# Optimization experiments

Hardware: AMD Instinct MI355X
Metric: run time of the kernel (lower is better)

The kernel has to match this reference:

```python
import jax, jax.numpy as jnp
import numpy as np

B, L, V, E, H2, M, OOV = 128, 400, 50000, 512, 1024, 1024, 50


def setup_inputs() -> dict:
    key = jax.random.key(0)
    ks = jax.random.split(key, 14)
    s = 0.02
    return {
        "y": jax.random.randint(ks[0], (B,), 0, V),
        "h": jax.random.normal(ks[1], (1, B, H2), jnp.float32),
        "memory_bank": jax.random.normal(ks[2], (B, L, M), jnp.float32),
        "src_mask": jnp.ones((B, L), jnp.float32),
        "max_num_oovs": OOV,
        "src_oov": jax.random.randint(ks[3], (B, L), 0, V + OOV),
        # learned parameters (PyTorch Linear y = x @ W + b with W stored [in, out])
        "emb": jax.random.normal(ks[4], (V, E), jnp.float32) * s,
        "W_ih": jax.random.normal(ks[5], (E, 3 * H2), jnp.float32) * s,   # GRU input weights (r|z|n)
        "W_hh": jax.random.normal(ks[6], (H2, 3 * H2), jnp.float32) * s,  # GRU hidden weights (r|z|n)
        "b_ih": jnp.zeros((3 * H2,), jnp.float32),
        "b_hh": jnp.zeros((3 * H2,), jnp.float32),
        "W_mem": jax.random.normal(ks[7], (M, H2), jnp.float32) * s,      # attention memory_project (no bias)
        "W_dec": jax.random.normal(ks[8], (H2, H2), jnp.float32) * s,     # attention decode_project
        "b_dec": jnp.zeros((H2,), jnp.float32),
        "v": jax.random.normal(ks[9], (H2,), jnp.float32) * s,            # attention score vector (no bias)
        "W_pgen": jax.random.normal(ks[10], (M + H2 + E, 1), jnp.float32) * s,
        "b_pgen": jnp.zeros((1,), jnp.float32),
        "W_v1": jax.random.normal(ks[11], (M + H2, H2), jnp.float32) * s,
        "b_v1": jnp.zeros((H2,), jnp.float32),
        "W_v2": jax.random.normal(ks[12], (H2, V), jnp.float32) * s,
        "b_v2": jnp.zeros((V,), jnp.float32),
    }


def reference(y, h, memory_bank, src_mask, max_num_oovs, src_oov,
              emb, W_ih, W_hh, b_ih, b_hh, W_mem, W_dec, b_dec, v,
              W_pgen, b_pgen, W_v1, b_v1, W_v2, b_v2):
    # --- embedding lookup (single decode step) ---
    y_emb = emb[y]                                    # [B, E]
    h0 = h[-1]                                        # [B, H2]

    # --- one-step GRU (PyTorch gate order r, z, n); dropout is identity (eval) ---
    gi = y_emb @ W_ih + b_ih                          # [B, 3*H2]
    gh = h0 @ W_hh + b_hh
    i_r, i_z, i_n = jnp.split(gi, 3, axis=-1)
    h_r, h_z, h_n = jnp.split(gh, 3, axis=-1)
    r = jax.nn.sigmoid(i_r + h_r)
    z = jax.nn.sigmoid(i_z + h_z)
    n = jnp.tanh(i_n + r * h_n)
    h_next = (1.0 - z) * n + z * h0                   # [B, H2]

    # --- concat (Bahdanau) attention with masked softmax ---
    enc_feat = jnp.einsum('blm,mh->blh', memory_bank, W_mem)   # [B, L, H2]
    dec_feat = h_next @ W_dec + b_dec                           # [B, H2]
    scores = jnp.tanh(enc_feat + dec_feat[:, None, :]) @ v     # [B, L]
    attn = jax.nn.softmax(scores, axis=1) * src_mask
    attn_dist = attn / attn.sum(axis=1, keepdims=True)         # renormalized masked softmax
    context = jnp.einsum('bl,blm->bm', attn_dist, memory_bank) # [B, M]

    # --- vocab distribution ---
    vd_in = jnp.concatenate([context, h_next], axis=1)          # [B, M+H2]
    logits = (vd_in @ W_v1 + b_v1) @ W_v2 + b_v2                # [B, V]
    vocab_dist = jax.nn.softmax(logits, axis=1)

    # --- generation gate ---
    pg_in = jnp.concatenate([context, h_next, y_emb], axis=1)   # [B, M+H2+E]
    p_gen = jax.nn.sigmoid(pg_in @ W_pgen + b_pgen)             # [B, 1]

    # --- copy mechanism: scatter attention mass into extended vocab ---
    vocab_dist_ = p_gen * vocab_dist
    attn_dist_ = (1.0 - p_gen) * attn_dist
    bsz = vocab_dist_.shape[0]
    if max_num_oovs > 0:
        vocab_dist_ = jnp.concatenate(
            [vocab_dist_, jnp.zeros((bsz, max_num_oovs), vocab_dist_.dtype)], axis=1)
    rows = jnp.arange(bsz)[:, None]
    final_dist = vocab_dist_.at[rows, src_oov].add(attn_dist_)  # [B, V+OOV]

    return final_dist, h_next[None], context, attn_dist, p_gen
```

## Files before the change

### kernel.cpp

```cpp
#include <hip/hip_runtime.h>

#define B_   128
#define L_   400
#define V_   50000
#define E_   512
#define H2_  1024
#define M_   1024
#define OOV_ 50
#define VE_  50050
#define BL_  51200

typedef __attribute__((ext_vector_type(8))) short short8;
typedef __attribute__((ext_vector_type(4))) float f32x4;

__device__ __forceinline__ unsigned short f2bf(float f){
  unsigned int u = __builtin_bit_cast(unsigned int, f);
  u = (u + 0x7FFFu + ((u >> 16) & 1u)) >> 16;
  return (unsigned short)u;
}
__device__ __forceinline__ float bf2f(unsigned short s){
  unsigned int u = ((unsigned int)s) << 16;
  return __builtin_bit_cast(float, u);
}

__device__ __forceinline__ void gl_lds16(const void* g, void* l){
  __builtin_amdgcn_global_load_lds(
      (const __attribute__((address_space(1))) unsigned int*)g,
      (__attribute__((address_space(3))) unsigned int*)l, 16, 0, 0);
}

__device__ __forceinline__ float wredsum(float v){
  #pragma unroll
  for (int o = 32; o > 0; o >>= 1) v += __shfl_xor(v, o);
  return v;
}
__device__ __forceinline__ float wredmax(float v){
  #pragma unroll
  for (int o = 32; o > 0; o >>= 1) v = fmaxf(v, __shfl_xor(v, o));
  return v;
}

__global__ void embed_gather_kernel(const int* __restrict__ y, const float* __restrict__ emb,
                                    float* __restrict__ yemb){
  int idx = blockIdx.x * 256 + threadIdx.x;
  int b  = idx >> 7;
  int c4 = (idx & 127) << 2;
  float4 v = *(const float4*)(emb + (size_t)y[b] * E_ + c4);
  *(float4*)(yemb + (size_t)b * E_ + c4) = v;
}

__global__ void mb_convert_kernel(const float* __restrict__ mb, unsigned char* __restrict__ mbT){
  int u = blockIdx.x * 256 + threadIdx.x;
  int gr  = u >> 7;
  int m16 = u & 127;
  const float* src = mb + (size_t)gr * 1024 + m16 * 8;
  float4 f0 = *(const float4*)src;
  float4 f1 = *(const float4*)(src + 4);
  uint4 w;
  w.x = (unsigned)f2bf(f0.x) | ((unsigned)f2bf(f0.y) << 16);
  w.y = (unsigned)f2bf(f0.z) | ((unsigned)f2bf(f0.w) << 16);
  w.z = (unsigned)f2bf(f1.x) | ((unsigned)f2bf(f1.y) << 16);
  w.w = (unsigned)f2bf(f1.z) | ((unsigned)f2bf(f1.w) << 16);
  int panel = gr >> 7, r = gr & 127;
  int ks = m16 >> 3, c16 = m16 & 7;
  size_t dst = (size_t)panel * 262144 + (size_t)ks * 16384
             + (size_t)((r * 128 + c16 * 16) ^ ((r & 7) << 4));
  *(uint4*)(mbT + dst) = w;
}

__global__ void wmem_transposeT_kernel(const float* __restrict__ W, unsigned char* __restrict__ WTt){
  __shared__ float tile[32][33];
  int n0 = blockIdx.x * 32, k0 = blockIdx.y * 32;
  int tx = threadIdx.x, ty = threadIdx.y;
  #pragma unroll
  for (int i = 0; i < 32; i += 8) tile[ty + i][tx] = W[(size_t)(k0 + ty + i) * H2_ + n0 + tx];
  __syncthreads();
  int id = ty * 32 + tx;
  if (id < 128){
    int nn = id & 31, k16 = id >> 5;
    int col = n0 + nn, kb = k0 + k16 * 8;
    uint4 w;
    w.x = (unsigned)f2bf(tile[k16*8+0][nn]) | ((unsigned)f2bf(tile[k16*8+1][nn]) << 16);
    w.y = (unsigned)f2bf(tile[k16*8+2][nn]) | ((unsigned)f2bf(tile[k16*8+3][nn]) << 16);
    w.z = (unsigned)f2bf(tile[k16*8+4][nn]) | ((unsigned)f2bf(tile[k16*8+5][nn]) << 16);
    w.w = (unsigned)f2bf(tile[k16*8+6][nn]) | ((unsigned)f2bf(tile[k16*8+7][nn]) << 16);
    int cpn = col >> 7, r = col & 127;
    int ks = kb >> 6, c16 = (kb & 63) >> 3;
    size_t dst = (size_t)cpn * 262144 + (size_t)ks * 16384
               + (size_t)((r * 128 + c16 * 16) ^ ((r & 7) << 4));
    *(uint4*)(WTt + dst) = w;
  }
}

__launch_bounds__(256)
__global__ void gemm128_kernel(const float* __restrict__ A, int lda,
                               const float* __restrict__ W, int ldw,
                               const float* __restrict__ bias,
                               float* __restrict__ C, int ldc,
                               int N, int kChunk, int addBias)
{
  int tid = threadIdx.x;
  int wv = tid >> 6, lane = tid & 63, lr = lane & 15, lhi = lane >> 4;
  int colBase = blockIdx.x * 128 + wv * 32;
  int colL[2];
  colL[0] = min(colBase + lr, N - 1);
  colL[1] = min(colBase + 16 + lr, N - 1);
  int k0 = blockIdx.y * kChunk;

  f32x4 zero = {0.f, 0.f, 0.f, 0.f};
  f32x4 acc[8][2];
  #pragma unroll
  for (int r = 0; r < 8; r++){ acc[r][0] = zero; acc[r][1] = zero; }

  int nks = kChunk >> 5;
  for (int ks = 0; ks < nks; ++ks){
    int k = k0 + ks * 32 + lhi * 8;
    short8 bf[2];
    #pragma unroll
    for (int cf = 0; cf < 2; cf++){
      #pragma unroll
      for (int j = 0; j < 8; j++)
        bf[cf][j] = (short)f2bf(W[(size_t)(k + j) * ldw + colL[cf]]);
    }
    #pragma unroll
    for (int rf = 0; rf < 8; rf++){
      const float* ap = A + (size_t)(rf * 16 + lr) * lda + k;
      float4 a0 = *(const float4*)ap;
      float4 a1 = *(const float4*)(ap + 4);
      short8 af;
      af[0]=(short)f2bf(a0.x); af[1]=(short)f2bf(a0.y); af[2]=(short)f2bf(a0.z); af[3]=(short)f2bf(a0.w);
      af[4]=(short)f2bf(a1.x); af[5]=(short)f2bf(a1.y); af[6]=(short)f2bf(a1.z); af[7]=(short)f2bf(a1.w);
      acc[rf][0] = __builtin_amdgcn_mfma_f32_16x16x32_bf16(af, bf[0], acc[rf][0], 0, 0, 0);
      acc[rf][1] = __builtin_amdgcn_mfma_f32_16x16x32_bf16(af, bf[1], acc[rf][1], 0, 0, 0);
    }
  }

  bool addB = addBias && (blockIdx.y == 0);
  #pragma unroll
  for (int cf = 0; cf < 2; cf++){
    int col = colBase + cf * 16 + lr;
    bool ok = col < N;
    float bv = addB ? bias[colL[cf]] : 0.f;
    #pragma unroll
    for (int rf = 0; rf < 8; rf++)
      #pragma unroll
      for (int i = 0; i < 4; i++){
        int row = rf * 16 + lhi * 4 + i;
        if (ok) atomicAdd(&C[(size_t)row * ldc + col], acc[rf][cf][i] + bv);
      }
  }
}

__launch_bounds__(256)
__global__ void gemm_v1_kernel(const float* __restrict__ A1, const float* __restrict__ A2,
                               const float* __restrict__ W,
                               const float* __restrict__ bias,
                               float* __restrict__ C, int N, int kChunk)
{
  int tid = threadIdx.x;
  int wv = tid >> 6, lane = tid & 63, lr = lane & 15, lhi = lane >> 4;
  int colBase = blockIdx.x * 128 + wv * 32;
  int halfY = gridDim.y >> 1;
  const float* Asrc = (blockIdx.y < halfY) ? A1 : A2;
  int yk = (blockIdx.y < halfY) ? blockIdx.y : (blockIdx.y - halfY);
  int k0 = yk * kChunk;
  int wk0 = blockIdx.y * kChunk;

  f32x4 zero = {0.f, 0.f, 0.f, 0.f};
  f32x4 acc[8][2];
  #pragma unroll
  for (int r = 0; r < 8; r++){ acc[r][0] = zero; acc[r][1] = zero; }

  int nks = kChunk >> 5;
  for (int ks = 0; ks < nks; ++ks){
    int k  = k0 + ks * 32 + lhi * 8;
    int wk = wk0 + ks * 32 + lhi * 8;
    short8 bf[2];
    #pragma unroll
    for (int cf = 0; cf < 2; cf++){
      #pragma unroll
      for (int j = 0; j < 8; j++)
        bf[cf][j] = (short)f2bf(W[(size_t)(wk + j) * H2_ + colBase + cf * 16 + lr]);
    }
    #pragma unroll
    for (int rf = 0; rf < 8; rf++){
      const float* ap = Asrc + (size_t)(rf * 16 + lr) * 1024 + k;
      float4 a0 = *(const float4*)ap;
      float4 a1 = *(const float4*)(ap + 4);
      short8 af;
      af[0]=(short)f2bf(a0.x); af[1]=(short)f2bf(a0.y); af[2]=(short)f2bf(a0.z); af[3]=(short)f2bf(a0.w);
      af[4]=(short)f2bf(a1.x); af[5]=(short)f2bf(a1.y); af[6]=(short)f2bf(a1.z); af[7]=(short)f2bf(a1.w);
      acc[rf][0] = __builtin_amdgcn_mfma_f32_16x16x32_bf16(af, bf[0], acc[rf][0], 0, 0, 0);
      acc[rf][1] = __builtin_amdgcn_mfma_f32_16x16x32_bf16(af, bf[1], acc[rf][1], 0, 0, 0);
    }
  }

  bool addB = (blockIdx.y == 0);
  #pragma unroll
  for (int cf = 0; cf < 2; cf++){
    int col = colBase + cf * 16 + lr;
    float bv = addB ? bias[col] : 0.f;
    #pragma unroll
    for (int rf = 0; rf < 8; rf++)
      #pragma unroll
      for (int i = 0; i < 4; i++){
        int row = rf * 16 + lhi * 4 + i;
        atomicAdd(&C[(size_t)row * H2_ + col], acc[rf][cf][i] + bv);
      }
  }
}

__launch_bounds__(256)
__global__ void gemm_bfA_kernel(const unsigned short* __restrict__ A,
                                const float* __restrict__ W,
                                const float* __restrict__ bias,
                                float* __restrict__ C0, float* __restrict__ C1,
                                int N, int kChunk)
{
  int tid = threadIdx.x;
  int wv = tid >> 6, lane = tid & 63, lr = lane & 15, lhi = lane >> 4;
  int colBase = blockIdx.x * 128 + wv * 32;
  int colL[2];
  colL[0] = min(colBase + lr, N - 1);
  colL[1] = min(colBase + 16 + lr, N - 1);
  int k0 = blockIdx.y * kChunk;
  float* Cw = (blockIdx.y == 0) ? C0 : C1;

  f32x4 zero = {0.f, 0.f, 0.f, 0.f};
  f32x4 acc[8][2];
  #pragma unroll
  for (int r = 0; r < 8; r++){ acc[r][0] = zero; acc[r][1] = zero; }

  int nks = kChunk >> 5;
  for (int ks = 0; ks < nks; ++ks){
    int k = k0 + ks * 32 + lhi * 8;
    short8 bf[2];
    #pragma unroll
    for (int cf = 0; cf < 2; cf++){
      #pragma unroll
      for (int j = 0; j < 8; j++)
        bf[cf][j] = (short)f2bf(W[(size_t)(k + j) * N + colL[cf]]);
    }
    #pragma unroll
    for (int rf = 0; rf < 8; rf++){
      short8 af = *(const short8*)(A + (size_t)(rf * 16 + lr) * 1024 + k);
      acc[rf][0] = __builtin_amdgcn_mfma_f32_16x16x32_bf16(af, bf[0], acc[rf][0], 0, 0, 0);
      acc[rf][1] = __builtin_amdgcn_mfma_f32_16x16x32_bf16(af, bf[1], acc[rf][1], 0, 0, 0);
    }
  }

  bool addB = (blockIdx.y == 0);
  #pragma unroll
  for (int cf = 0; cf < 2; cf++){
    int col = colBase + cf * 16 + lr;
    bool ok = col < N;
    float bv = addB ? bias[colL[cf]] : 0.f;
    #pragma unroll
    for (int rf = 0; rf < 8; rf++)
      #pragma unroll
      for (int i = 0; i < 4; i++){
        int row = rf * 16 + lhi * 4 + i;
        if (ok) Cw[(size_t)row * V_ + col] = acc[rf][cf][i] + bv;
      }
  }
}

__global__ void gru_gates_kernel(const float* __restrict__ gi, const float* __restrict__ gh,
                                 const float* __restrict__ bih, const float* __restrict__ bhh,
                                 const float* __restrict__ h0, float* __restrict__ hn){
  int idx = blockIdx.x * 256 + threadIdx.x;
  int b = idx >> 10, j = idx & 1023;
  const float* gib = gi + (size_t)b * 3072;
  const float* ghb = gh + (size_t)b * 3072;
  float ir = gib[j]        + bih[j],        hr = ghb[j]        + bhh[j];
  float iz = gib[j + 1024] + bih[j + 1024], hz = ghb[j + 1024] + bhh[j + 1024];
  float in_= gib[j + 2048] + bih[j + 2048], hnv= ghb[j + 2048] + bhh[j + 2048];
  float r = 1.f / (1.f + __expf(-(ir + hr)));
  float z = 1.f / (1.f + __expf(-(iz + hz)));
  float n = tanhf(in_ + r * hnv);
  hn[idx] = (1.f - z) * n + z * h0[idx];
}

__launch_bounds__(512, 3)
__global__ void scores_kernel(const unsigned char* __restrict__ mbT,
                              const unsigned char* __restrict__ WTt,
                              const float* __restrict__ dec, const float* __restrict__ vvec,
                              float* __restrict__ scr)
{
  __shared__ __align__(16) unsigned char LDSm[65536];
  const int tid = threadIdx.x, lane = tid & 63;
  const int wv = tid >> 6, lr = lane & 15, lhi = lane >> 4;
  const int wru = wv >> 2, wcu = wv & 3;

  int p = blockIdx.x;
  int lid = (p & 7) * 400 + (p >> 3);
  int rp = lid >> 3, cp = lid & 7;
  int r0 = rp << 7;

  int wvu = __builtin_amdgcn_readfirstlane(wv);
  const unsigned char* seg = (wvu < 4 ? mbT + (size_t)rp * 262144
                                      : WTt + (size_t)cp * 262144)
                             + (wvu & 3) * 4096 + lane * 16;
  const int segLds = (wvu & 3) * 4096 + (wvu < 4 ? 0 : 16384);

  int aoff[4], boff[2];
  #pragma unroll
  for (int rf = 0; rf < 4; rf++){
    int row = wru * 64 + rf * 16 + lr;
    aoff[rf] = (row * 128 + lhi * 16) ^ ((row & 7) << 4);
  }
  #pragma unroll
  for (int cf = 0; cf < 2; cf++){
    int col = wcu * 32 + cf * 16 + lr;
    boff[cf] = ((col * 128 + lhi * 16) ^ ((col & 7) << 4)) + 16384;
  }

  f32x4 zero = {0.f, 0.f, 0.f, 0.f};
  f32x4 acc[4][2];
  #pragma unroll
  for (int rf = 0; rf < 4; rf++){ acc[rf][0] = zero; acc[rf][1] = zero; }

  #pragma unroll
  for (int j = 0; j < 4; j++)
    gl_lds16(seg + j * 1024, &LDSm[segLds + j * 1024]);

  #pragma unroll 1
  for (int t = 0; t < 16; ++t){
    const int cur = (t & 1) << 15;
    if (t < 15){
      const unsigned char* s = seg + (size_t)(t + 1) * 16384;
      const int nb = ((t + 1) & 1) << 15;
      #pragma unroll
      for (int j = 0; j < 4; j++)
        gl_lds16(s + j * 1024, &LDSm[nb + segLds + j * 1024]);
      asm volatile("s_waitcnt vmcnt(4)" ::: "memory");
    } else {
      asm volatile("s_waitcnt vmcnt(0)" ::: "memory");
    }
    __builtin_amdgcn_sched_barrier(0);
    __builtin_amdgcn_s_barrier();
    __builtin_amdgcn_sched_barrier(0);
    #pragma unroll
    for (int k2 = 0; k2 < 2; k2++){
      short8 af[4], bfr[2];
      #pragma unroll
      for (int rf = 0; rf < 4; rf++) af[rf]  = *(const short8*)&LDSm[cur + (aoff[rf] ^ (k2 << 6))];
      #pragma unroll
      for (int cf = 0; cf < 2; cf++) bfr[cf] = *(const short8*)&LDSm[cur + (boff[cf] ^ (k2 << 6))];
      __builtin_amdgcn_s_setprio(1);
      #pragma unroll
      for (int rf = 0; rf < 4; rf++)
        #pragma unroll
        for (int cf = 0; cf < 2; cf++)
          acc[rf][cf] = __builtin_amdgcn_mfma_f32_16x16x32_bf16(af[rf], bfr[cf], acc[rf][cf], 0, 0, 0);
      __builtin_amdgcn_s_setprio(0);
    }
    __builtin_amdgcn_sched_barrier(0);
    asm volatile("s_waitcnt lgkmcnt(0)" ::: "memory");
    __builtin_amdgcn_s_barrier();
    __builtin_amdgcn_sched_barrier(0);
  }

  int colb = (cp << 7) + wcu * 32 + lr;
  float vv0 = vvec[colb], vv1 = vvec[colb + 16];
  #pragma unroll
  for (int rf = 0; rf < 4; rf++){
    #pragma unroll
    for (int i = 0; i < 4; i++){
      int grow = r0 + wru * 64 + rf * 16 + lhi * 4 + i;
      int bb = grow / 400;
      const float* dp = dec + (size_t)bb * 1024 + colb;
      float x0 = acc[rf][0][i] + dp[0];
      float x1 = acc[rf][1][i] + dp[16];
      float part = (1.f - 2.f / (__expf(2.f * x0) + 1.f)) * vv0
                 + (1.f - 2.f / (__expf(2.f * x1) + 1.f)) * vv1;
      part += __shfl_xor(part, 1);
      part += __shfl_xor(part, 2);
      part += __shfl_xor(part, 4);
      part += __shfl_xor(part, 8);
      if (lr == 0) atomicAdd(&scr[grow], part);
    }
  }
}

__global__ void attn_softmax_kernel(const float* __restrict__ scores, const float* __restrict__ mask,
                                    float* __restrict__ attn){
  int b = blockIdx.x, t = threadIdx.x;
  int wv = t >> 6, lane = t & 63;
  __shared__ float red[4];
  float s0 = (t < 400)       ? scores[b * 400 + t]       : -1e30f;
  float s1 = (t + 256 < 400) ? scores[b * 400 + t + 256] : -1e30f;
  float m = wredmax(fmaxf(s0, s1));
  if (lane == 0) red[wv] = m;
  __syncthreads();
  float M = fmaxf(fmaxf(red[0], red[1]), fmaxf(red[2], red[3]));
  __syncthreads();
  float e0 = (t < 400)       ? __expf(s0 - M) * mask[b * 400 + t]       : 0.f;
  float e1 = (t + 256 < 400) ? __expf(s1 - M) * mask[b * 400 + t + 256] : 0.f;
  float s = wredsum(e0 + e1);
  if (lane == 0) red[wv] = s;
  __syncthreads();
  float inv = 1.f / (red[0] + red[1] + red[2] + red[3]);
  if (t < 400)       attn[b * 400 + t]       = e0 * inv;
  if (t + 256 < 400) attn[b * 400 + t + 256] = e1 * inv;
}

__launch_bounds__(256)
__global__ void context_kernel(const float* __restrict__ attn, const unsigned char* __restrict__ mbT,
                               float* __restrict__ ctx){
  int b = blockIdx.y, lc = blockIdx.x, t = threadIdx.x;
  int u = t & 127;
  int half = t >> 7;
  __shared__ float a[100];
  if (t < 100) a[t] = attn[b * 400 + lc * 100 + t];
  __syncthreads();
  int ks = u >> 3, c16 = u & 7;
  float s[8];
  #pragma unroll
  for (int j = 0; j < 8; j++) s[j] = 0.f;
  for (int l = half; l < 100; l += 2){
    int gr = b * 400 + lc * 100 + l;
    int panel = gr >> 7, r = gr & 127;
    const unsigned char* pp = mbT + (size_t)panel * 262144 + (size_t)ks * 16384
                              + (size_t)((r * 128 + c16 * 16) ^ ((r & 7) << 4));
    short8 v = *(const short8*)pp;
    float al = a[l];
    #pragma unroll
    for (int j = 0; j < 8; j++) s[j] += al * bf2f((unsigned short)v[j]);
  }
  float* cp = ctx + (size_t)b * M_ + u * 8;
  #pragma unroll
  for (int j = 0; j < 8; j++) atomicAdd(cp + j, s[j]);
}

__global__ void pgen_kernel(const float* __restrict__ ctx, const float* __restrict__ hn,
                            const float* __restrict__ yemb,
                            const float* __restrict__ Wp, const float* __restrict__ bp,
                            float* __restrict__ pg){
  int b = blockIdx.x, t = threadIdx.x, wv = t >> 6, lane = t & 63;
  __shared__ float red[4];
  float s = 0.f;
  for (int i = t; i < 1024; i += 256) s += ctx[(size_t)b * 1024 + i] * Wp[i];
  for (int i = t; i < 1024; i += 256) s += hn[(size_t)b * 1024 + i] * Wp[1024 + i];
  for (int i = t; i < 512;  i += 256) s += yemb[(size_t)b * 512 + i] * Wp[2048 + i];
  s = wredsum(s);
  if (lane == 0) red[wv] = s;
  __syncthreads();
  if (t == 0){
    float S = red[0] + red[1] + red[2] + red[3] + bp[0];
    pg[b] = 1.f / (1.f + __expf(-S));
  }
}

__global__ void hid2bf_kernel(const float* __restrict__ hid, unsigned short* __restrict__ hb){
  int idx = blockIdx.x * 256 + threadIdx.x;
  float4 v = *(const float4*)(hid + (size_t)idx * 4);
  ushort2 p0 = {f2bf(v.x), f2bf(v.y)};
  ushort2 p1 = {f2bf(v.z), f2bf(v.w)};
  *(ushort2*)(hb + (size_t)idx * 4)     = p0;
  *(ushort2*)(hb + (size_t)idx * 4 + 2) = p1;
}

__global__ void vocab_softmax_kernel(float* __restrict__ lg0, const float* __restrict__ lg1,
                                     const float* __restrict__ pg,
                                     const float* __restrict__ attn, const int* __restrict__ soov,
                                     float* __restrict__ fin){
  int b = blockIdx.x, t = threadIdx.x, wv = t >> 6, lane = t & 63;
  __shared__ float redm[16], reds[16];
  float* l0 = lg0 + (size_t)b * V_;
  const float* l1 = lg1 + (size_t)b * V_;
  float m = -1e30f, s = 0.f;
  for (int i = t; i < V_; i += 1024){
    float l = l0[i] + l1[i];
    l0[i] = l;
    float mn = fmaxf(m, l);
    s = s * __expf(m - mn) + __expf(l - mn);
    m = mn;
  }
  #pragma unroll
  for (int o = 32; o > 0; o >>= 1){
    float mo = __shfl_xor(m, o), so = __shfl_xor(s, o);
    float mn = fmaxf(m, mo);
    s = s * __expf(m - mn) + so * __expf(mo - mn);
    m = mn;
  }
  if (lane == 0){ redm[wv] = m; reds[wv] = s; }
  __syncthreads();
  float M = -1e30f;
  #pragma unroll
  for (int w = 0; w < 16; w++) M = fmaxf(M, redm[w]);
  float S = 0.f;
  #pragma unroll
  for (int w = 0; w < 16; w++) S += reds[w] * __expf(redm[w] - M);
  float pgb = pg[b];
  float scale = pgb / S;
  float* fb = fin + (size_t)b * VE_;
  for (int i = t; i < V_; i += 1024) fb[i] = __expf(l0[i] - M) * scale;
  for (int i = V_ + t; i < VE_; i += 1024) fb[i] = 0.f;
  __syncthreads();
  float om = 1.f - pgb;
  if (t < 400) atomicAdd(&fb[soov[b * 400 + t]], om * attn[b * 400 + t]);
}

extern "C" void kernel_launch(void* const* d_in, const int* in_sizes, int n_in,
                              void* d_out, int out_size, void* d_ws, size_t ws_size,
                              hipStream_t stream)
{
  const int*   y     = (const int*)  d_in[0];
  const float* hin   = (const float*)d_in[1];
  const float* mb    = (const float*)d_in[2];
  const float* mask  = (const float*)d_in[3];
  const int*   soov  = (const int*)  d_in[5];
  const float* emb   = (const float*)d_in[6];
  const float* W_ih  = (const float*)d_in[7];
  const float* W_hh  = (const float*)d_in[8];
  const float* b_ih  = (const float*)d_in[9];
  const float* b_hh  = (const float*)d_in[10];
  const float* W_mem = (const float*)d_in[11];
  const float* W_dec = (const float*)d_in[12];
  const float* b_dec = (const float*)d_in[13];
  const float* vvec  = (const float*)d_in[14];
  const float* W_pg  = (const float*)d_in[15];
  const float* b_pg  = (const float*)d_in[16];
  const float* W_v1  = (const float*)d_in[17];
  const float* b_v1  = (const float*)d_in[18];
  const float* W_v2  = (const float*)d_in[19];
  const float* b_v2  = (const float*)d_in[20];

  float* out   = (float*)d_out;
  float* fin   = out;
  float* hnext = out + (size_t)B_ * VE_;
  float* ctx   = hnext + (size_t)B_ * H2_;
  float* attn  = ctx + (size_t)B_ * M_;
  float* pg    = attn + (size_t)B_ * L_;

  float* ws   = (float*)d_ws;
  float* yemb = ws;
  float* gi   = ws + 65536;
  float* gh   = gi + 393216;
  float* dec  = gh + 393216;
  float* scr  = dec + 131072;
  float* hid  = scr + 51200;
  float* lg0  = hid + 131072;
  unsigned short* hidbf = (unsigned short*)(lg0 + 6400000);
  unsigned char*  WTt   = (unsigned char*)(hidbf + 131072);
  unsigned char*  mbT   = WTt + 2097152;
  float* lg1  = (float*)mbT;

  hipMemsetAsync(gi, 0, (size_t)(393216 + 393216 + 131072 + 51200) * 4, stream);
  hipMemsetAsync(hid, 0, (size_t)131072 * 4, stream);
  hipMemsetAsync(ctx, 0, (size_t)B_ * M_ * 4, stream);

  embed_gather_kernel<<<64, 256, 0, stream>>>(y, emb, yemb);
  wmem_transposeT_kernel<<<dim3(32, 32), dim3(32, 8), 0, stream>>>(W_mem, WTt);
  mb_convert_kernel<<<25600, 256, 0, stream>>>(mb, mbT);

  gemm128_kernel<<<dim3(24, 2), 256, 0, stream>>>(yemb, E_,  W_ih, 3 * H2_, nullptr, gi, 3 * H2_, 3 * H2_, 256, 0);
  gemm128_kernel<<<dim3(24, 4), 256, 0, stream>>>(hin,  H2_, W_hh, 3 * H2_, nullptr, gh, 3 * H2_, 3 * H2_, 256, 0);
  gru_gates_kernel<<<512, 256, 0, stream>>>(gi, gh, b_ih, b_hh, hin, hnext);
  gemm128_kernel<<<dim3(8, 4), 256, 0, stream>>>(hnext, H2_, W_dec, H2_, b_dec, dec, H2_, H2_, 256, 1);

  scores_kernel<<<3200, 512, 0, stream>>>(mbT, WTt, dec, vvec, scr);
  attn_softmax_kernel<<<128, 256, 0, stream>>>(scr, mask, attn);
  context_kernel<<<dim3(4, 128), 256, 0, stream>>>(attn, mbT, ctx);

  pgen_kernel<<<128, 256, 0, stream>>>(ctx, hnext, yemb, W_pg, b_pg, pg);
  gemm_v1_kernel<<<dim3(8, 8), 256, 0, stream>>>(ctx, hnext, W_v1, b_v1, hid, H2_, 256);
  hid2bf_kernel<<<128, 256, 0, stream>>>(hid, hidbf);
  gemm_bfA_kernel<<<dim3(391, 2), 256, 0, stream>>>(hidbf, W_v2, b_v2, lg0, lg1, V_, 512);

  vocab_softmax_kernel<<<128, 1024, 0, stream>>>(lg0, lg1, pg, attn, soov, fin);
}
```

Baseline: 598.0 us.

## Enlarge scores GEMM tile to 256x256 and fuse prologue kernels and memsets

The attention scores GEMM moves from 128x128 to 256x256 output tiles with 128 KB of double-buffered LDS, eight-load prefetch stages and 8x4 MFMA accumulators per wave. This roughly halves global/L2 traffic per FLOP but allows fewer resident blocks per CU and launches only 800 blocks. Separately, the memory-bank conversion, W_mem transpose, embedding gather and three memsets are merged into one multi-role launch. The two GRU input/hidden GEMMs share a single launch to cut launch and idle-gap overhead.

```diff
diff --git a/kernel.cpp b/kernel.cpp
--- a/kernel.cpp
+++ b/kernel.cpp
@@ -40,60 +40,71 @@
   return v;
 }
 
-__global__ void embed_gather_kernel(const int* __restrict__ y, const float* __restrict__ emb,
-                                    float* __restrict__ yemb){
-  int idx = blockIdx.x * 256 + threadIdx.x;
-  int b  = idx >> 7;
-  int c4 = (idx & 127) << 2;
-  float4 v = *(const float4*)(emb + (size_t)y[b] * E_ + c4);
-  *(float4*)(yemb + (size_t)b * E_ + c4) = v;
-}
-
-__global__ void mb_convert_kernel(const float* __restrict__ mb, unsigned char* __restrict__ mbT){
-  int u = blockIdx.x * 256 + threadIdx.x;
-  int gr  = u >> 7;
-  int m16 = u & 127;
-  const float* src = mb + (size_t)gr * 1024 + m16 * 8;
-  float4 f0 = *(const float4*)src;
-  float4 f1 = *(const float4*)(src + 4);
-  uint4 w;
-  w.x = (unsigned)f2bf(f0.x) | ((unsigned)f2bf(f0.y) << 16);
-  w.y = (unsigned)f2bf(f0.z) | ((unsigned)f2bf(f0.w) << 16);
-  w.z = (unsigned)f2bf(f1.x) | ((unsigned)f2bf(f1.y) << 16);
-  w.w = (unsigned)f2bf(f1.z) | ((unsigned)f2bf(f1.w) << 16);
-  int panel = gr >> 7, r = gr & 127;
-  int ks = m16 >> 3, c16 = m16 & 7;
-  size_t dst = (size_t)panel * 262144 + (size_t)ks * 16384
-             + (size_t)((r * 128 + c16 * 16) ^ ((r & 7) << 4));
-  *(uint4*)(mbT + dst) = w;
-}
-
-__global__ void wmem_transposeT_kernel(const float* __restrict__ W, unsigned char* __restrict__ WTt){
+__global__ void phase1_kernel(const float* __restrict__ mb, unsigned char* __restrict__ mbT,
+                              const float* __restrict__ Wm, unsigned char* __restrict__ WTt,
+                              const int* __restrict__ y, const float* __restrict__ emb,
+                              float* __restrict__ yemb, float* __restrict__ zeroA,
+                              float* __restrict__ ctx)
+{
   __shared__ float tile[32][33];
-  int n0 = blockIdx.x * 32, k0 = blockIdx.y * 32;
-  int tx = threadIdx.x, ty = threadIdx.y;
-  #pragma unroll
-  for (int i = 0; i < 32; i += 8) tile[ty + i][tx] = W[(size_t)(k0 + ty + i) * H2_ + n0 + tx];
-  __syncthreads();
-  int id = ty * 32 + tx;
-  if (id < 128){
-    int nn = id & 31, k16 = id >> 5;
-    int col = n0 + nn, kb = k0 + k16 * 8;
+  int bid = blockIdx.x, t = threadIdx.x;
+  if (bid < 25600){
+    int u = bid * 256 + t;
+    int gr  = u >> 7;
+    int m16 = u & 127;
+    const float* src = mb + (size_t)gr * 1024 + m16 * 8;
+    float4 f0 = *(const float4*)src;
+    float4 f1 = *(const float4*)(src + 4);
     uint4 w;
-    w.x = (unsigned)f2bf(tile[k16*8+0][nn]) | ((unsigned)f2bf(tile[k16*8+1][nn]) << 16);
-    w.y = (unsigned)f2bf(tile[k16*8+2][nn]) | ((unsigned)f2bf(tile[k16*8+3][nn]) << 16);
-    w.z = (unsigned)f2bf(tile[k16*8+4][nn]) | ((unsigned)f2bf(tile[k16*8+5][nn]) << 16);
-    w.w = (unsigned)f2bf(tile[k16*8+6][nn]) | ((unsigned)f2bf(tile[k16*8+7][nn]) << 16);
-    int cpn = col >> 7, r = col & 127;
-    int ks = kb >> 6, c16 = (kb & 63) >> 3;
-    size_t dst = (size_t)cpn * 262144 + (size_t)ks * 16384
+    w.x = (unsigned)f2bf(f0.x) | ((unsigned)f2bf(f0.y) << 16);
+    w.y = (unsigned)f2bf(f0.z) | ((unsigned)f2bf(f0.w) << 16);
+    w.z = (unsigned)f2bf(f1.x) | ((unsigned)f2bf(f1.y) << 16);
+    w.w = (unsigned)f2bf(f1.z) | ((unsigned)f2bf(f1.w) << 16);
+    int panel = gr >> 7, r = gr & 127;
+    int ks = m16 >> 3, c16 = m16 & 7;
+    size_t dst = (size_t)panel * 262144 + (size_t)ks * 16384
                + (size_t)((r * 128 + c16 * 16) ^ ((r & 7) << 4));
-    *(uint4*)(WTt + dst) = w;
-  }
-}
-
-__launch_bounds__(256)
-__global__ void gemm128_kernel(const float* __restrict__ A, int lda,
+    *(uint4*)(mbT + dst) = w;
+  } else if (bid < 26624){
+    int b2 = bid - 25600;
+    int n0 = (b2 & 31) * 32, k0 = (b2 >> 5) * 32;
+    int tx = t & 31, ty = t >> 5;
+    #pragma unroll
+    for (int i = 0; i < 32; i += 8) tile[ty + i][tx] = Wm[(size_t)(k0 + ty + i) * H2_ + n0 + tx];
+    __syncthreads();
+    if (t < 128){
+      int nn = t & 31, k16 = t >> 5;
+      int col = n0 + nn, kb = k0 + k16 * 8;
+      uint4 w;
+      w.x = (unsigned)f2bf(tile[k16*8+0][nn]) | ((unsigned)f2bf(tile[k16*8+1][nn]) << 16);
+      w.y = (unsigned)f2bf(tile[k16*8+2][nn]) | ((unsigned)f2bf(tile[k16*8+3][nn]) << 16);
+      w.z = (unsigned)f2bf(tile[k16*8+4][nn]) | ((unsigned)f2bf(tile[k16*8+5][nn]) << 16);
+      w.w = (unsigned)f2bf(tile[k16*8+6][nn]) | ((unsigned)f2bf(tile[k16*8+7][nn]) << 16);
+      int cpn = col >> 7, r = col & 127;
+      int ks = kb >> 6, c16 = (kb & 63) >> 3;
+      size_t dst = (size_t)cpn * 262144 + (size_t)ks * 16384
+                 + (size_t)((r * 128 + c16 * 16) ^ ((r & 7) << 4));
+      *(uint4*)(WTt + dst) = w;
+    }
+  } else if (bid < 26688){
+    int idx = (bid - 26624) * 256 + t;
+    int b  = idx >> 7;
+    int c4 = (idx & 127) << 2;
+    float4 v = *(const float4*)(emb + (size_t)y[b] * E_ + c4);
+    *(float4*)(yemb + (size_t)b * E_ + c4) = v;
+  } else if (bid < 27762){
+    int u = (bid - 26688) * 256 + t;
+    float4 z = {0.f, 0.f, 0.f, 0.f};
+    *(float4*)(zeroA + (size_t)u * 4) = z;
+  } else {
+    int u = (bid - 27762) * 256 + t;
+    float4 z = {0.f, 0.f, 0.f, 0.f};
+    *(float4*)(ctx + (size_t)u * 4) = z;
+  }
+}
+
+__device__ __forceinline__ void gemm128_body(int bx, int by,
+                               const float* __restrict__ A, int lda,
                                const float* __restrict__ W, int ldw,
                                const float* __restrict__ bias,
                                float* __restrict__ C, int ldc,
@@ -101,11 +112,11 @@
 {
   int tid = threadIdx.x;
   int wv = tid >> 6, lane = tid & 63, lr = lane & 15, lhi = lane >> 4;
-  int colBase = blockIdx.x * 128 + wv * 32;
+  int colBase = bx * 128 + wv * 32;
   int colL[2];
   colL[0] = min(colBase + lr, N - 1);
   colL[1] = min(colBase + 16 + lr, N - 1);
-  int k0 = blockIdx.y * kChunk;
+  int k0 = by * kChunk;
 
   f32x4 zero = {0.f, 0.f, 0.f, 0.f};
   f32x4 acc[8][2];
@@ -135,7 +146,7 @@
     }
   }
 
-  bool addB = addBias && (blockIdx.y == 0);
+  bool addB = addBias && (by == 0);
   #pragma unroll
   for (int cf = 0; cf < 2; cf++){
     int col = colBase + cf * 16 + lr;
@@ -148,6 +159,28 @@
         int row = rf * 16 + lhi * 4 + i;
         if (ok) atomicAdd(&C[(size_t)row * ldc + col], acc[rf][cf][i] + bv);
       }
+  }
+}
+
+__launch_bounds__(256)
+__global__ void gemm128_kernel(const float* __restrict__ A, int lda,
+                               const float* __restrict__ W, int ldw,
+                               const float* __restrict__ bias,
+                               float* __restrict__ C, int ldc,
+                               int N, int kChunk, int addBias){
+  gemm128_body(blockIdx.x, blockIdx.y, A, lda, W, ldw, bias, C, ldc, N, kChunk, addBias);
+}
+
+__launch_bounds__(256)
+__global__ void gigh_kernel(const float* __restrict__ yemb, const float* __restrict__ hin,
+                            const float* __restrict__ W_ih, const float* __restrict__ W_hh,
+                            float* __restrict__ gi, float* __restrict__ gh){
+  int bid = blockIdx.x;
+  if (bid < 48)
+    gemm128_body(bid % 24, bid / 24, yemb, E_,  W_ih, 3 * H2_, nullptr, gi, 3 * H2_, 3 * H2_, 256, 0);
+  else {
+    int b2 = bid - 48;
+    gemm128_body(b2 % 24, b2 / 24, hin, H2_, W_hh, 3 * H2_, nullptr, gh, 3 * H2_, 3 * H2_, 256, 0);
   }
 }
 
@@ -281,59 +314,62 @@
   hn[idx] = (1.f - z) * n + z * h0[idx];
 }
 
-__launch_bounds__(512, 3)
+__launch_bounds__(512, 2)
 __global__ void scores_kernel(const unsigned char* __restrict__ mbT,
                               const unsigned char* __restrict__ WTt,
                               const float* __restrict__ dec, const float* __restrict__ vvec,
                               float* __restrict__ scr)
 {
-  __shared__ __align__(16) unsigned char LDSm[65536];
+  __shared__ __align__(16) unsigned char LDSm[131072];
   const int tid = threadIdx.x, lane = tid & 63;
   const int wv = tid >> 6, lr = lane & 15, lhi = lane >> 4;
   const int wru = wv >> 2, wcu = wv & 3;
 
   int p = blockIdx.x;
-  int lid = (p & 7) * 400 + (p >> 3);
-  int rp = lid >> 3, cp = lid & 7;
-  int r0 = rp << 7;
+  int lid = (p & 7) * 100 + (p >> 3);
+  int rp = lid >> 2, cp = lid & 3;
+  int r0 = rp << 8;
 
   int wvu = __builtin_amdgcn_readfirstlane(wv);
-  const unsigned char* seg = (wvu < 4 ? mbT + (size_t)rp * 262144
-                                      : WTt + (size_t)cp * 262144)
-                             + (wvu & 3) * 4096 + lane * 16;
-  const int segLds = (wvu & 3) * 4096 + (wvu < 4 ? 0 : 16384);
-
-  int aoff[4], boff[2];
-  #pragma unroll
-  for (int rf = 0; rf < 4; rf++){
-    int row = wru * 64 + rf * 16 + lr;
+  int idx4 = wvu & 3, half = idx4 >> 1, sub = idx4 & 1;
+  const unsigned char* seg = (wvu < 4 ? mbT + (size_t)(2 * rp + half) * 262144
+                                      : WTt + (size_t)(2 * cp + half) * 262144)
+                             + sub * 8192 + lane * 16;
+  const int segLds = (wvu < 4 ? 0 : 32768) + idx4 * 8192;
+
+  int aoff[8], boff[4];
+  #pragma unroll
+  for (int rf = 0; rf < 8; rf++){
+    int row = wru * 128 + rf * 16 + lr;
     aoff[rf] = (row * 128 + lhi * 16) ^ ((row & 7) << 4);
   }
   #pragma unroll
-  for (int cf = 0; cf < 2; cf++){
-    int col = wcu * 32 + cf * 16 + lr;
-    boff[cf] = ((col * 128 + lhi * 16) ^ ((col & 7) << 4)) + 16384;
+  for (int cf = 0; cf < 4; cf++){
+    int col = wcu * 64 + cf * 16 + lr;
+    boff[cf] = 32768 + ((col * 128 + lhi * 16) ^ ((col & 7) << 4));
   }
 
   f32x4 zero = {0.f, 0.f, 0.f, 0.f};
-  f32x4 acc[4][2];
-  #pragma unroll
-  for (int rf = 0; rf < 4; rf++){ acc[rf][0] = zero; acc[rf][1] = zero; }
-
-  #pragma unroll
-  for (int j = 0; j < 4; j++)
+  f32x4 acc[8][4];
+  #pragma unroll
+  for (int rf = 0; rf < 8; rf++)
+    #pragma unroll
+    for (int cf = 0; cf < 4; cf++) acc[rf][cf] = zero;
+
+  #pragma unroll
+  for (int j = 0; j < 8; j++)
     gl_lds16(seg + j * 1024, &LDSm[segLds + j * 1024]);
 
   #pragma unroll 1
   for (int t = 0; t < 16; ++t){
-    const int cur = (t & 1) << 15;
+    const int cur = (t & 1) << 16;
     if (t < 15){
       const unsigned char* s = seg + (size_t)(t + 1) * 16384;
-      const int nb = ((t + 1) & 1) << 15;
-      #pragma unroll
-      for (int j = 0; j < 4; j++)
+      const int nb = ((t + 1) & 1) << 16;
+      #pragma unroll
+      for (int j = 0; j < 8; j++)
         gl_lds16(s + j * 1024, &LDSm[nb + segLds + j * 1024]);
-      asm volatile("s_waitcnt vmcnt(4)" ::: "memory");
+      asm volatile("s_waitcnt vmcnt(8)" ::: "memory");
     } else {
       asm volatile("s_waitcnt vmcnt(0)" ::: "memory");
     }
@@ -342,16 +378,16 @@
     __builtin_amdgcn_sched_barrier(0);
     #pragma unroll
     for (int k2 = 0; k2 < 2; k2++){
-      short8 af[4], bfr[2];
-      #pragma unroll
-      for (int rf = 0; rf < 4; rf++) af[rf]  = *(const short8*)&LDSm[cur + (aoff[rf] ^ (k2 << 6))];
-      #pragma unroll
-      for (int cf = 0; cf < 2; cf++) bfr[cf] = *(const short8*)&LDSm[cur + (boff[cf] ^ (k2 << 6))];
+      short8 af[8], bfr[4];
+      #pragma unroll
+      for (int rf = 0; rf < 8; rf++) af[rf]  = *(const short8*)&LDSm[cur + (aoff[rf] ^ (k2 << 6))];
+      #pragma unroll
+      for (int cf = 0; cf < 4; cf++) bfr[cf] = *(const short8*)&LDSm[cur + (boff[cf] ^ (k2 << 6))];
       __builtin_amdgcn_s_setprio(1);
       #pragma unroll
-      for (int rf = 0; rf < 4; rf++)
+      for (int rf = 0; rf < 8; rf++)
         #pragma unroll
-        for (int cf = 0; cf < 2; cf++)
+        for (int cf = 0; cf < 4; cf++)
           acc[rf][cf] = __builtin_amdgcn_mfma_f32_16x16x32_bf16(af[rf], bfr[cf], acc[rf][cf], 0, 0, 0);
       __builtin_amdgcn_s_setprio(0);
     }
@@ -361,19 +397,23 @@
     __builtin_amdgcn_sched_barrier(0);
   }
 
-  int colb = (cp << 7) + wcu * 32 + lr;
-  float vv0 = vvec[colb], vv1 = vvec[colb + 16];
-  #pragma unroll
-  for (int rf = 0; rf < 4; rf++){
+  int colb = (cp << 8) + wcu * 64 + lr;
+  float vv0 = vvec[colb], vv1 = vvec[colb + 16], vv2 = vvec[colb + 32], vv3 = vvec[colb + 48];
+  #pragma unroll
+  for (int rf = 0; rf < 8; rf++){
     #pragma unroll
     for (int i = 0; i < 4; i++){
-      int grow = r0 + wru * 64 + rf * 16 + lhi * 4 + i;
+      int grow = r0 + wru * 128 + rf * 16 + lhi * 4 + i;
       int bb = grow / 400;
       const float* dp = dec + (size_t)bb * 1024 + colb;
       float x0 = acc[rf][0][i] + dp[0];
       float x1 = acc[rf][1][i] + dp[16];
+      float x2 = acc[rf][2][i] + dp[32];
+      float x3 = acc[rf][3][i] + dp[48];
       float part = (1.f - 2.f / (__expf(2.f * x0) + 1.f)) * vv0
-                 + (1.f - 2.f / (__expf(2.f * x1) + 1.f)) * vv1;
+                 + (1.f - 2.f / (__expf(2.f * x1) + 1.f)) * vv1
+                 + (1.f - 2.f / (__expf(2.f * x2) + 1.f)) * vv2
+                 + (1.f - 2.f / (__expf(2.f * x3) + 1.f)) * vv3;
       part += __shfl_xor(part, 1);
       part += __shfl_xor(part, 2);
       part += __shfl_xor(part, 4);
@@ -547,20 +587,13 @@
   unsigned char*  mbT   = WTt + 2097152;
   float* lg1  = (float*)mbT;
 
-  hipMemsetAsync(gi, 0, (size_t)(393216 + 393216 + 131072 + 51200) * 4, stream);
-  hipMemsetAsync(hid, 0, (size_t)131072 * 4, stream);
-  hipMemsetAsync(ctx, 0, (size_t)B_ * M_ * 4, stream);
-
-  embed_gather_kernel<<<64, 256, 0, stream>>>(y, emb, yemb);
-  wmem_transposeT_kernel<<<dim3(32, 32), dim3(32, 8), 0, stream>>>(W_mem, WTt);
-  mb_convert_kernel<<<25600, 256, 0, stream>>>(mb, mbT);
-
-  gemm128_kernel<<<dim3(24, 2), 256, 0, stream>>>(yemb, E_,  W_ih, 3 * H2_, nullptr, gi, 3 * H2_, 3 * H2_, 256, 0);
-  gemm128_kernel<<<dim3(24, 4), 256, 0, stream>>>(hin,  H2_, W_hh, 3 * H2_, nullptr, gh, 3 * H2_, 3 * H2_, 256, 0);
+  phase1_kernel<<<27890, 256, 0, stream>>>(mb, mbT, W_mem, WTt, y, emb, yemb, gi, ctx);
+
+  gigh_kernel<<<144, 256, 0, stream>>>(yemb, hin, W_ih, W_hh, gi, gh);
   gru_gates_kernel<<<512, 256, 0, stream>>>(gi, gh, b_ih, b_hh, hin, hnext);
   gemm128_kernel<<<dim3(8, 4), 256, 0, stream>>>(hnext, H2_, W_dec, H2_, b_dec, dec, H2_, H2_, 256, 1);
 
-  scores_kernel<<<3200, 512, 0, stream>>>(mbT, WTt, dec, vvec, scr);
+  scores_kernel<<<800, 512, 0, stream>>>(mbT, WTt, dec, vvec, scr);
   attn_softmax_kernel<<<128, 256, 0, stream>>>(scr, mask, attn);
   context_kernel<<<dim3(4, 128), 256, 0, stream>>>(attn, mbT, ctx);
 
```

Measured after the change: 577.5 us. -3.4%, faster.
